# Optimization experiments

Measured on AMD Instinct MI355X. Metric: run time of the kernel, lower is better.

The kernel has to match this reference:

```python
import jax, jax.numpy as jnp
import numpy as np

B, N, C = 2, 4096, 1024
H, D = 16, 64
EPS = 1e-6


def setup_inputs() -> dict:
    key = jax.random.key(0)
    k1, k2, k3 = jax.random.split(key, 3)
    hidden_states = jax.random.normal(k1, (B, N, C), dtype=jnp.float32)
    # realistic RoPE tables: inv_freq over half-dim, duplicated to full head_dim
    half = D // 2
    inv_freq = 1.0 / (10000.0 ** (jnp.arange(half, dtype=jnp.float32) / half))
    t = jnp.arange(N, dtype=jnp.float32)
    freqs = jnp.outer(t, inv_freq)                     # [N, D/2]
    emb = jnp.concatenate([freqs, freqs], axis=-1)     # [N, D]
    cos, sin = jnp.cos(emb), jnp.sin(emb)
    Wqkv = jax.random.normal(k2, (C, 3 * C), dtype=jnp.float32) * (C ** -0.5)
    Wout = jax.random.normal(k3, (C, C), dtype=jnp.float32) * (C ** -0.5)
    gq = jnp.ones((D,), dtype=jnp.float32)
    gk = jnp.ones((D,), dtype=jnp.float32)
    return {"hidden_states": hidden_states, "cos": cos, "sin": sin,
            "Wqkv": Wqkv, "Wout": Wout, "gq": gq, "gk": gk}


def _rmsnorm(x, g):
    # normalize over last dim (head_dim)
    var = jnp.mean(jnp.square(x), axis=-1, keepdims=True)
    return x * jax.lax.rsqrt(var + EPS) * g


def _rotate_half(x):
    x1, x2 = jnp.split(x, 2, axis=-1)
    return jnp.concatenate([-x2, x1], axis=-1)


def reference(hidden_states, cos, sin, Wqkv, Wout, gq, gk):
    b, n, c = hidden_states.shape
    qkv = (hidden_states @ Wqkv).reshape(b, n, 3, H, D)
    qkv = jnp.transpose(qkv, (2, 0, 3, 1, 4))
    q, k, v = qkv[0], qkv[1], qkv[2]
    # per-head RMSNorm on q/k
    q = _rmsnorm(q, gq)
    k = _rmsnorm(k, gk)
    # RoPE: cos/sin [N,D] broadcast to [B,H,N,D]
    q = q * cos + _rotate_half(q) * sin
    k = k * cos + _rotate_half(k) * sin
    # full SDPA (flex_attention with no block_mask/score_mod)
    scale = D ** -0.5
    scores = jnp.einsum("bhqd,bhkd->bhqk", q, k) * scale
    probs = jax.nn.softmax(scores, axis=-1)
    attn = jnp.einsum("bhqk,bhkd->bhqd", probs, v)
    attn = jnp.transpose(attn, (0, 2, 1, 3)).reshape(b, n, c)
    return attn @ Wout
```

## Files before the change

### kernel.cpp

```cpp
#include <hip/hip_runtime.h>
#include <hip/hip_bf16.h>
#include <stdint.h>

#define LOG2E 1.44269504088896340736f

typedef __attribute__((ext_vector_type(8))) short short8;
typedef __attribute__((ext_vector_type(4))) float f32x4;
typedef __attribute__((ext_vector_type(16))) float f32x16;
typedef __attribute__((ext_vector_type(4))) unsigned short us4;

static __device__ __forceinline__ float bf2f(unsigned short u) {
    union { unsigned int i; float f; } v; v.i = ((unsigned int)u) << 16; return v.f;
}
static __device__ __forceinline__ unsigned short f2bf(float f) {
    __hip_bfloat16 h = __float2bfloat16(f);
    union { __hip_bfloat16 h; unsigned short u; } v; v.h = h; return v.u;
}

#define GLL(gsrc, ldst) \
    __builtin_amdgcn_global_load_lds((const __attribute__((address_space(1))) unsigned int*)(gsrc), \
                                     (__attribute__((address_space(3))) unsigned int*)(ldst), 16, 0, 0)

__global__ __launch_bounds__(256) void conv_bf16(const float4* __restrict__ in,
                                                 us4* __restrict__ out, int n4) {
    int i = blockIdx.x * blockDim.x + threadIdx.x;
    int stride = gridDim.x * blockDim.x;
    for (; i < n4; i += stride) {
        float4 v = in[i];
        us4 o;
        o[0] = f2bf(v.x); o[1] = f2bf(v.y); o[2] = f2bf(v.z); o[3] = f2bf(v.w);
        out[i] = o;
    }
}

__global__ __launch_bounds__(256) void transpose_w(const float* __restrict__ W,
                                                   unsigned short* __restrict__ WT,
                                                   int K, int M) {
    __shared__ unsigned short T[64][65];
    int m0 = blockIdx.x * 64, k0 = blockIdx.y * 64;
    int r = threadIdx.x >> 2, q = (threadIdx.x & 3) * 16;
    const float4* src = (const float4*)(W + (size_t)(k0 + r) * M + m0 + q);
#pragma unroll
    for (int j = 0; j < 4; j++) {
        float4 v = src[j];
        T[r][q + j * 4 + 0] = f2bf(v.x);
        T[r][q + j * 4 + 1] = f2bf(v.y);
        T[r][q + j * 4 + 2] = f2bf(v.z);
        T[r][q + j * 4 + 3] = f2bf(v.w);
    }
    __syncthreads();
    unsigned short tmp[16];
#pragma unroll
    for (int j = 0; j < 16; j++) tmp[j] = T[q + j][r];
    unsigned short* dst = WT + (size_t)(m0 + r) * K + k0 + q;
    *(short8*)dst = *(const short8*)tmp;
    *(short8*)(dst + 8) = *(const short8*)(tmp + 8);
}

__device__ __forceinline__ void gemm_core(const unsigned short* __restrict__ A,
                                          const unsigned short* __restrict__ Bt,
                                          int brow, int bcol,
                                          unsigned short* As, unsigned short* Bs,
                                          f32x4 (&acc)[4][4]) {
    const int tid = threadIdx.x;
    const int w = tid >> 6, lane = tid & 63;
    const int g = lane >> 4, c = lane & 15;
    const int wr = (w >> 1) * 64, wc = (w & 1) * 64;

    for (int k0 = 0; k0 < 1024; k0 += 64) {
        __syncthreads();
#pragma unroll
        for (int i = 0; i < 4; i++) {
            int slot = i * 256 + tid;
            int row = slot >> 3, sub = slot & 7;
            int koff = k0 + ((sub ^ (row & 7)) << 3);
            GLL(A + (size_t)(brow + row) * 1024 + koff, As + (size_t)(i * 256 + w * 64) * 8);
            GLL(Bt + (size_t)(bcol + row) * 1024 + koff, Bs + (size_t)(i * 256 + w * 64) * 8);
        }
        __syncthreads();
#pragma unroll
        for (int kc = 0; kc < 2; kc++) {
            short8 a[4], b[4];
#pragma unroll
            for (int f = 0; f < 4; f++) {
                int rowA = wr + f * 16 + c;
                a[f] = *(const short8*)(As + (size_t)(rowA * 8 + ((kc * 4 + g) ^ (rowA & 7))) * 8);
                int rowB = wc + f * 16 + c;
                b[f] = *(const short8*)(Bs + (size_t)(rowB * 8 + ((kc * 4 + g) ^ (rowB & 7))) * 8);
            }
#pragma unroll
            for (int fi = 0; fi < 4; fi++)
#pragma unroll
                for (int fj = 0; fj < 4; fj++)
                    acc[fi][fj] = __builtin_amdgcn_mfma_f32_16x16x32_bf16(a[fi], b[fj], acc[fi][fj], 0, 0, 0);
        }
    }
}

__global__ __launch_bounds__(256) void gemm_qkv(const unsigned short* __restrict__ A,
                                                const unsigned short* __restrict__ Bt,
                                                unsigned short* __restrict__ qkv,
                                                unsigned short* __restrict__ vt) {
    __shared__ unsigned short As[128 * 64];
    __shared__ unsigned short Bs[128 * 64];
    const int tid = threadIdx.x;
    const int lane = tid & 63, w = tid >> 6;
    const int g = lane >> 4, c = lane & 15;
    const int brow = blockIdx.x * 128, bcol = blockIdx.y * 128;
    const int wr = (w >> 1) * 64, wc = (w & 1) * 64;

    f32x4 acc[4][4];
#pragma unroll
    for (int i = 0; i < 4; i++)
#pragma unroll
        for (int j = 0; j < 4; j++) acc[i][j] = (f32x4){0.f, 0.f, 0.f, 0.f};

    gemm_core(A, Bt, brow, bcol, As, Bs, acc);

    if (bcol < 2048) {
#pragma unroll
        for (int fi = 0; fi < 4; fi++) {
            int row = brow + wr + fi * 16 + g * 4;
#pragma unroll
            for (int fj = 0; fj < 4; fj++) {
                int col = bcol + wc + fj * 16 + c;
#pragma unroll
                for (int r = 0; r < 4; r++)
                    qkv[(size_t)(row + r) * 2048 + col] = f2bf(acc[fi][fj][r]);
            }
        }
    } else {
        int b = brow >> 12;
        int nbase = (brow & 4095) + wr;
#pragma unroll
        for (int fi = 0; fi < 4; fi++) {
            int n0 = nbase + fi * 16 + g * 4;
#pragma unroll
            for (int fj = 0; fj < 4; fj++) {
                int hd = bcol - 2048 + wc + fj * 16 + c;
                us4 pk;
#pragma unroll
                for (int r = 0; r < 4; r++) pk[r] = f2bf(acc[fi][fj][r]);
                *(us4*)(vt + (size_t)(b * 1024 + hd) * 4096 + n0) = pk;
            }
        }
    }
}

__global__ __launch_bounds__(256) void gemm_out(const unsigned short* __restrict__ A,
                                                const unsigned short* __restrict__ Bt,
                                                float* __restrict__ C) {
    __shared__ unsigned short As[128 * 64];
    __shared__ unsigned short Bs[128 * 64];
    const int tid = threadIdx.x;
    const int lane = tid & 63, w = tid >> 6;
    const int g = lane >> 4, c = lane & 15;
    const int brow = blockIdx.x * 128, bcol = blockIdx.y * 128;
    const int wr = (w >> 1) * 64, wc = (w & 1) * 64;

    f32x4 acc[4][4];
#pragma unroll
    for (int i = 0; i < 4; i++)
#pragma unroll
        for (int j = 0; j < 4; j++) acc[i][j] = (f32x4){0.f, 0.f, 0.f, 0.f};

    gemm_core(A, Bt, brow, bcol, As, Bs, acc);

#pragma unroll
    for (int fi = 0; fi < 4; fi++) {
        int row = brow + wr + fi * 16 + g * 4;
#pragma unroll
        for (int fj = 0; fj < 4; fj++) {
            int col = bcol + wc + fj * 16 + c;
#pragma unroll
            for (int r = 0; r < 4; r++)
                C[(size_t)(row + r) * 1024 + col] = acc[fi][fj][r];
        }
    }
}

__global__ __launch_bounds__(256) void norm_rope(unsigned short* __restrict__ qkv,
                                                 const float* __restrict__ cosb,
                                                 const float* __restrict__ sinb,
                                                 const float* __restrict__ gq,
                                                 const float* __restrict__ gk) {
    int u = blockIdx.x * 4 + (threadIdx.x >> 6);
    int lane = threadIdx.x & 63;
    int t = u >> 5, rest = u & 31, h = rest >> 1, qk = rest & 1;
    int n = t & 4095;
    unsigned short* p = qkv + (size_t)t * 2048 + qk * 1024 + h * 64 + lane;
    float x = bf2f(*p);
    float ss = x * x;
#pragma unroll
    for (int m = 1; m < 64; m <<= 1) ss += __shfl_xor(ss, m, 64);
    float rr = rsqrtf(ss * 0.015625f + 1e-6f);
    float xn = x * rr * (qk ? gk[lane] : gq[lane]);
    float other = __shfl_xor(xn, 32, 64);
    float cv = cosb[n * 64 + lane], sv = sinb[n * 64 + lane];
    float rh = (lane < 32) ? -other : other;
    *p = f2bf(xn * cv + rh * sv);
}

__global__ __launch_bounds__(256, 4) void attn_fwd(const unsigned short* __restrict__ qkv,
                                                   const unsigned short* __restrict__ vt,
                                                   unsigned short* __restrict__ attn) {
    __shared__ unsigned short Ks[2][4096];
    __shared__ unsigned short Vs[2][4096];
    const int tid = threadIdx.x;
    const int w = tid >> 6, lane = tid & 63;
    const int c31 = lane & 31, hi = lane >> 5;

    int logical = (blockIdx.x & 7) * 128 + (blockIdx.x >> 3);
    const int bh = logical >> 5, qt = logical & 31;
    const int b = bh >> 4, h = bh & 15;
    const size_t tokbase = (size_t)b * 4096;
    const int q0 = qt * 128 + w * 32;

    short8 qf[4];
#pragma unroll
    for (int sl = 0; sl < 4; sl++)
        qf[sl] = *(const short8*)(qkv + (tokbase + q0 + c31) * 2048 + h * 64 + sl * 16 + hi * 8);

    f32x16 o[2];
#pragma unroll
    for (int ds = 0; ds < 2; ds++)
#pragma unroll
        for (int r = 0; r < 16; r++) o[ds][r] = 0.f;
    float l_run = 0.f;

    const float SCL = 0.125f * LOG2E;
    const float NB = -9.0f * LOG2E;

#define STAGE_KV(bi, kv0)                                                                     \
    {                                                                                          \
        _Pragma("unroll") for (int i = 0; i < 2; i++) {                                        \
            int s2 = i * 4 + w;                                                                \
            GLL(qkv + (tokbase + (kv0) + lane) * 2048 + 1024 + h * 64 + s2 * 8,                \
                &Ks[bi][(size_t)s2 * 512]);                                                    \
            GLL(vt + ((size_t)(bh * 64 + lane)) * 4096 + (kv0) + s2 * 8,                       \
                &Vs[bi][(size_t)s2 * 512]);                                                    \
        }                                                                                      \
    }

    STAGE_KV(0, 0);
    int cur = 0;

    for (int t = 0; t < 64; t++) {
        __syncthreads();
        if (t < 63) STAGE_KV(cur ^ 1, (t + 1) * 64);

        short8 kf[2][4];
#pragma unroll
        for (int m = 0; m < 2; m++)
#pragma unroll
            for (int sl = 0; sl < 4; sl++)
                kf[m][sl] = *(const short8*)&Ks[cur][(size_t)(((sl * 2 + hi) * 64) + m * 32 + c31) * 8];

        f32x16 sacc[2];
        __builtin_amdgcn_s_setprio(1);
#pragma unroll
        for (int m = 0; m < 2; m++) {
            f32x16 a;
#pragma unroll
            for (int r = 0; r < 16; r++) a[r] = 0.f;
#pragma unroll
            for (int sl = 0; sl < 4; sl++)
                a = __builtin_amdgcn_mfma_f32_32x32x16_bf16(kf[m][sl], qf[sl], a, 0, 0, 0);
            sacc[m] = a;
        }
        __builtin_amdgcn_s_setprio(0);

        short8 pf[4];
        {
#pragma unroll
            for (int m = 0; m < 2; m++)
#pragma unroll
                for (int r = 0; r < 16; r++)
                    sacc[m][r] = __builtin_amdgcn_exp2f(fmaf(sacc[m][r], SCL, NB));

            f32x16 t16;
#pragma unroll
            for (int r = 0; r < 16; r++) t16[r] = sacc[0][r] + sacc[1][r];
#pragma unroll
            for (int st = 8; st > 0; st >>= 1)
#pragma unroll
                for (int j = 0; j < st; j++) t16[j] += t16[j + st];
            {
                union { float f; unsigned int u; } sa, sb;
                sa.f = t16[0]; sb.f = t16[0];
                asm("v_permlane32_swap_b32 %0, %1" : "+v"(sa.u), "+v"(sb.u));
                l_run += t16[0] + (hi ? sa.f : sb.f);
            }

#pragma unroll
            for (int m = 0; m < 2; m++) {
                unsigned int q2[8];
#pragma unroll
                for (int w8 = 0; w8 < 8; w8++) {
                    unsigned int r_;
                    asm("v_cvt_pk_bf16_f32 %0, %1, %2"
                        : "=v"(r_)
                        : "v"(sacc[m][2 * w8]), "v"(sacc[m][2 * w8 + 1]));
                    q2[w8] = r_;
                }
                asm("v_permlane32_swap_b32 %0, %1" : "+v"(q2[0]), "+v"(q2[2]));
                asm("v_permlane32_swap_b32 %0, %1" : "+v"(q2[1]), "+v"(q2[3]));
                asm("v_permlane32_swap_b32 %0, %1" : "+v"(q2[4]), "+v"(q2[6]));
                asm("v_permlane32_swap_b32 %0, %1" : "+v"(q2[5]), "+v"(q2[7]));
                union { unsigned int u[4]; short8 s; } f0, f1;
                f0.u[0] = q2[0]; f0.u[1] = q2[1]; f0.u[2] = q2[2]; f0.u[3] = q2[3];
                f1.u[0] = q2[4]; f1.u[1] = q2[5]; f1.u[2] = q2[6]; f1.u[3] = q2[7];
                pf[2 * m] = f0.s;
                pf[2 * m + 1] = f1.s;
            }
        }

        __builtin_amdgcn_s_setprio(1);
#pragma unroll
        for (int ds = 0; ds < 2; ds++)
#pragma unroll
            for (int kvs = 0; kvs < 4; kvs++) {
                short8 vf = *(const short8*)&Vs[cur][(size_t)(((kvs * 2 + hi) * 64) + ds * 32 + c31) * 8];
                o[ds] = __builtin_amdgcn_mfma_f32_32x32x16_bf16(vf, pf[kvs], o[ds], 0, 0, 0);
            }
        __builtin_amdgcn_s_setprio(0);
        cur ^= 1;
    }

    {
        float inv = 1.f / l_run;
        int token = q0 + c31;
#pragma unroll
        for (int ds = 0; ds < 2; ds++)
#pragma unroll
            for (int rb = 0; rb < 4; rb++) {
                us4 pk;
#pragma unroll
                for (int j = 0; j < 4; j++) pk[j] = f2bf(o[ds][rb * 4 + j] * inv);
                *(us4*)(attn + (tokbase + token) * 1024 + h * 64 + ds * 32 + rb * 8 + hi * 4) = pk;
            }
    }
#undef STAGE_KV
}

extern "C" void kernel_launch(void* const* d_in, const int* in_sizes, int n_in,
                              void* d_out, int out_size, void* d_ws, size_t ws_size,
                              hipStream_t stream) {
    const float* hs   = (const float*)d_in[0];
    const float* cosb = (const float*)d_in[1];
    const float* sinb = (const float*)d_in[2];
    const float* wqkv = (const float*)d_in[3];
    const float* wout = (const float*)d_in[4];
    const float* gq   = (const float*)d_in[5];
    const float* gk   = (const float*)d_in[6];
    float* out = (float*)d_out;

    char* ws = (char*)d_ws;
    unsigned short* Xb    = (unsigned short*)(ws);
    unsigned short* WqkvT = (unsigned short*)(ws + 16777216);
    unsigned short* WoutT = (unsigned short*)(ws + 23068672);
    unsigned short* qkv   = (unsigned short*)(ws + 25165824);
    unsigned short* vt    = (unsigned short*)(ws + 58720256);
    unsigned short* attn  = (unsigned short*)(ws + 75497472);

    conv_bf16<<<4096, 256, 0, stream>>>((const float4*)hs, (us4*)Xb, (8192 * 1024) / 4);
    transpose_w<<<dim3(48, 16), 256, 0, stream>>>(wqkv, WqkvT, 1024, 3072);
    transpose_w<<<dim3(16, 16), 256, 0, stream>>>(wout, WoutT, 1024, 1024);
    gemm_qkv<<<dim3(64, 24), 256, 0, stream>>>(Xb, WqkvT, qkv, vt);
    norm_rope<<<65536, 256, 0, stream>>>(qkv, cosb, sinb, gq, gk);
    attn_fwd<<<1024, 256, 0, stream>>>(qkv, vt, attn);
    gemm_out<<<dim3(64, 8), 256, 0, stream>>>(attn, WoutT, out);
}
```

Before: 400.4 us.

## Fuse RMSNorm and RoPE into QKV GEMM epilogue and swizzle GEMM block order

Removes the separate norm_rope kernel and applies the per-head RMSNorm and rotary embedding directly on the fp32 accumulators in the QKV GEMM epilogue, using a 16-lane shuffle reduction over each 64-wide head held by a wave. This avoids a full read/write pass over the Q/K buffer and one kernel launch, and also skips a bf16 round trip before normalization. Both GEMMs also switch to a 1D grid with a block-index swizzle meant to spread consecutive blocks across XCDs for better L2 locality. The epilogue now reads cos/sin per row with strided loads and carries more register pressure.

```diff
diff --git a/kernel.cpp b/kernel.cpp
--- a/kernel.cpp
+++ b/kernel.cpp
@@ -100,13 +100,19 @@
 __global__ __launch_bounds__(256) void gemm_qkv(const unsigned short* __restrict__ A,
                                                 const unsigned short* __restrict__ Bt,
                                                 unsigned short* __restrict__ qkv,
-                                                unsigned short* __restrict__ vt) {
+                                                unsigned short* __restrict__ vt,
+                                                const float* __restrict__ cosb,
+                                                const float* __restrict__ sinb,
+                                                const float* __restrict__ gq,
+                                                const float* __restrict__ gk) {
     __shared__ unsigned short As[128 * 64];
     __shared__ unsigned short Bs[128 * 64];
     const int tid = threadIdx.x;
     const int lane = tid & 63, w = tid >> 6;
     const int g = lane >> 4, c = lane & 15;
-    const int brow = blockIdx.x * 128, bcol = blockIdx.y * 128;
+    int bid = blockIdx.x;
+    int swz = (bid & 7) * 192 + (bid >> 3);
+    const int brow = (swz & 63) * 128, bcol = (swz >> 6) * 128;
     const int wr = (w >> 1) * 64, wc = (w & 1) * 64;
 
     f32x4 acc[4][4];
@@ -118,15 +124,50 @@
     gemm_core(A, Bt, brow, bcol, As, Bs, acc);
 
     if (bcol < 2048) {
+        const int qk = (bcol + wc) >> 10;
+        const float* gvec = qk ? gk : gq;
+        float gv[4];
+#pragma unroll
+        for (int fj = 0; fj < 4; fj++) gv[fj] = gvec[fj * 16 + c];
+
 #pragma unroll
         for (int fi = 0; fi < 4; fi++) {
-            int row = brow + wr + fi * 16 + g * 4;
-#pragma unroll
-            for (int fj = 0; fj < 4; fj++) {
-                int col = bcol + wc + fj * 16 + c;
-#pragma unroll
-                for (int r = 0; r < 4; r++)
-                    qkv[(size_t)(row + r) * 2048 + col] = f2bf(acc[fi][fj][r]);
+            float ss[4];
+#pragma unroll
+            for (int r = 0; r < 4; r++) {
+                float s = 0.f;
+#pragma unroll
+                for (int fj = 0; fj < 4; fj++) { float x = acc[fi][fj][r]; s = fmaf(x, x, s); }
+                ss[r] = s;
+            }
+#pragma unroll
+            for (int m = 1; m < 16; m <<= 1)
+#pragma unroll
+                for (int r = 0; r < 4; r++) ss[r] += __shfl_xor(ss[r], m, 64);
+            int rowbase = brow + wr + fi * 16 + g * 4;
+#pragma unroll
+            for (int r = 0; r < 4; r++) {
+                float rr = rsqrtf(ss[r] * 0.015625f + 1e-6f);
+                int row = rowbase + r;
+                int n = row & 4095;
+                float xn[4];
+#pragma unroll
+                for (int fj = 0; fj < 4; fj++) xn[fj] = acc[fi][fj][r] * rr * gv[fj];
+                float cv[4], sv[4];
+#pragma unroll
+                for (int fj = 0; fj < 4; fj++) {
+                    cv[fj] = cosb[n * 64 + fj * 16 + c];
+                    sv[fj] = sinb[n * 64 + fj * 16 + c];
+                }
+                float o0 = xn[0] * cv[0] - xn[2] * sv[0];
+                float o1 = xn[1] * cv[1] - xn[3] * sv[1];
+                float o2 = xn[2] * cv[2] + xn[0] * sv[2];
+                float o3 = xn[3] * cv[3] + xn[1] * sv[3];
+                size_t base = (size_t)row * 2048 + bcol + wc + c;
+                qkv[base + 0]  = f2bf(o0);
+                qkv[base + 16] = f2bf(o1);
+                qkv[base + 32] = f2bf(o2);
+                qkv[base + 48] = f2bf(o3);
             }
         }
     } else {
@@ -155,7 +196,9 @@
     const int tid = threadIdx.x;
     const int lane = tid & 63, w = tid >> 6;
     const int g = lane >> 4, c = lane & 15;
-    const int brow = blockIdx.x * 128, bcol = blockIdx.y * 128;
+    int bid = blockIdx.x;
+    int swz = (bid & 7) * 64 + (bid >> 3);
+    const int brow = (swz & 63) * 128, bcol = (swz >> 6) * 128;
     const int wr = (w >> 1) * 64, wc = (w & 1) * 64;
 
     f32x4 acc[4][4];
@@ -177,28 +220,6 @@
                 C[(size_t)(row + r) * 1024 + col] = acc[fi][fj][r];
         }
     }
-}
-
-__global__ __launch_bounds__(256) void norm_rope(unsigned short* __restrict__ qkv,
-                                                 const float* __restrict__ cosb,
-                                                 const float* __restrict__ sinb,
-                                                 const float* __restrict__ gq,
-                                                 const float* __restrict__ gk) {
-    int u = blockIdx.x * 4 + (threadIdx.x >> 6);
-    int lane = threadIdx.x & 63;
-    int t = u >> 5, rest = u & 31, h = rest >> 1, qk = rest & 1;
-    int n = t & 4095;
-    unsigned short* p = qkv + (size_t)t * 2048 + qk * 1024 + h * 64 + lane;
-    float x = bf2f(*p);
-    float ss = x * x;
-#pragma unroll
-    for (int m = 1; m < 64; m <<= 1) ss += __shfl_xor(ss, m, 64);
-    float rr = rsqrtf(ss * 0.015625f + 1e-6f);
-    float xn = x * rr * (qk ? gk[lane] : gq[lane]);
-    float other = __shfl_xor(xn, 32, 64);
-    float cv = cosb[n * 64 + lane], sv = sinb[n * 64 + lane];
-    float rh = (lane < 32) ? -other : other;
-    *p = f2bf(xn * cv + rh * sv);
 }
 
 __global__ __launch_bounds__(256, 4) void attn_fwd(const unsigned short* __restrict__ qkv,
@@ -366,8 +387,7 @@
     conv_bf16<<<4096, 256, 0, stream>>>((const float4*)hs, (us4*)Xb, (8192 * 1024) / 4);
     transpose_w<<<dim3(48, 16), 256, 0, stream>>>(wqkv, WqkvT, 1024, 3072);
     transpose_w<<<dim3(16, 16), 256, 0, stream>>>(wout, WoutT, 1024, 1024);
-    gemm_qkv<<<dim3(64, 24), 256, 0, stream>>>(Xb, WqkvT, qkv, vt);
-    norm_rope<<<65536, 256, 0, stream>>>(qkv, cosb, sinb, gq, gk);
+    gemm_qkv<<<1536, 256, 0, stream>>>(Xb, WqkvT, qkv, vt, cosb, sinb, gq, gk);
     attn_fwd<<<1024, 256, 0, stream>>>(qkv, vt, attn);
-    gemm_out<<<dim3(64, 8), 256, 0, stream>>>(attn, WoutT, out);
-}
+    gemm_out<<<512, 256, 0, stream>>>(attn, WoutT, out);
+}
```

New measurement: 388.1 us. 1.03x faster.
